# Optimization experiments

Measured on AMD Instinct MI355X. Metric: run time of the kernel, lower is better.

Reference implementation:

```python
import jax, jax.numpy as jnp
import numpy as np

D_MODEL = 1024
N_HEAD = 16
DK = D_MODEL // N_HEAD


def setup_inputs() -> dict:
    key = jax.random.key(0)
    ks = jax.random.split(key, 9)
    s = 1.0 / np.sqrt(D_MODEL)
    x = jax.random.normal(ks[0], (2, 2048, D_MODEL), dtype=jnp.float32)
    def lin(kw, kb):
        W = jax.random.uniform(kw, (D_MODEL, D_MODEL), minval=-s, maxval=s, dtype=jnp.float32)
        b = jax.random.uniform(kb, (D_MODEL,), minval=-s, maxval=s, dtype=jnp.float32)
        return W, b
    Wq, bq = lin(ks[1], ks[2])
    Wk, bk = lin(ks[3], ks[4])
    Wv, bv = lin(ks[5], ks[6])
    Wo, bo = lin(ks[7], ks[8])
    return {"x": x, "Wq": Wq, "bq": bq, "Wk": Wk, "bk": bk,
            "Wv": Wv, "bv": bv, "Wo": Wo, "bo": bo}


def reference(x, Wq, bq, Wk, bk, Wv, bv, Wo, bo):
    B, T, _ = x.shape
    # nn.Linear: x @ W.T + b; reshape to (B, H, T, dk)
    def proj(W, b):
        y = x @ W.T + b
        return y.reshape(B, T, N_HEAD, DK).transpose(0, 2, 1, 3)
    Q = proj(Wq, bq)
    K = proj(Wk, bk)
    V = proj(Wv, bv)
    scores = jnp.einsum('bhqd,bhkd->bhqk', Q, K) / jnp.sqrt(jnp.float32(DK))
    attn = jax.nn.softmax(scores, axis=-1)
    out = jnp.einsum('bhqk,bhkd->bhqd', attn, V)
    out = out.transpose(0, 2, 1, 3).reshape(B, T, D_MODEL)
    return out @ Wo.T + bo
```

## Files before the change

### kernel.cpp

```cpp
#include <hip/hip_runtime.h>
#include <hip/hip_bf16.h>
#include <cstdint>

typedef unsigned short u16;
typedef __attribute__((ext_vector_type(8))) __bf16 bf16x8;
typedef __attribute__((ext_vector_type(8))) short s16x8;
typedef __attribute__((ext_vector_type(4))) short s16x4;
typedef __attribute__((ext_vector_type(4))) float f32x4;
typedef __attribute__((ext_vector_type(4))) unsigned u32x4;

#define T_SEQ 2048
#define D_MODEL 1024
#define MROWS 4096
#define QSCALE (0.125f * 1.44269504088896f)

__device__ __forceinline__ u16 f2bf(float f) {
  unsigned u = __builtin_bit_cast(unsigned, f);
  u += 0x7fffu + ((u >> 16) & 1u);
  return (u16)(u >> 16);
}

__device__ __forceinline__ unsigned cvt_pk_bf16(float lo, float hi) {
  unsigned r;
  asm("v_cvt_pk_bf16_f32 %0, %1, %2" : "=v"(r) : "v"(lo), "v"(hi));
  return r;
}

__device__ __forceinline__ void plswap(unsigned& a, unsigned& b) {
  asm("v_permlane32_swap_b32 %0, %1" : "+v"(a), "+v"(b));
  asm("v_permlane16_swap_b32 %0, %1" : "+v"(a), "+v"(b));
}

__device__ __forceinline__ void gld_lds16(const void* g, void* l) {
  __builtin_amdgcn_global_load_lds(
      (__attribute__((address_space(1))) void*)(uintptr_t)(g),
      (__attribute__((address_space(3))) void*)(uintptr_t)(l), 16, 0, 0);
}

__device__ __forceinline__ f32x4 mfma16(s16x8 a, s16x8 b, f32x4 c) {
  return __builtin_amdgcn_mfma_f32_16x16x32_bf16(
      __builtin_bit_cast(bf16x8, a), __builtin_bit_cast(bf16x8, b), c, 0, 0, 0);
}

__global__ __launch_bounds__(256) void cvt5(
    const float* __restrict__ x,
    const float* __restrict__ w0, const float* __restrict__ w1,
    const float* __restrict__ w2, const float* __restrict__ w3,
    u16* __restrict__ dx, u16* __restrict__ dw0, u16* __restrict__ dw1,
    u16* __restrict__ dw2, u16* __restrict__ dw3) {
  const int NX = (MROWS * D_MODEL) / 4;
  const int NW = (D_MODEL * D_MODEL) / 4;
  int i = blockIdx.x * 256 + threadIdx.x;
  const float* s;
  u16* d;
  int off;
  if (i < NX) {
    s = x; d = dx; off = i;
  } else {
    int j = i - NX;
    int r = j >> 18;
    off = j & (NW - 1);
    if (r == 0) { s = w0; d = dw0; }
    else if (r == 1) { s = w1; d = dw1; }
    else if (r == 2) { s = w2; d = dw2; }
    else { s = w3; d = dw3; }
  }
  float4 v = ((const float4*)s)[off];
  uint2 o;
  o.x = cvt_pk_bf16(v.x, v.y);
  o.y = cvt_pk_bf16(v.z, v.w);
  ((uint2*)d)[off] = o;
}

__global__ __launch_bounds__(512, 2) void gemm_qkv(const u16* __restrict__ A,
    const u16* __restrict__ Wf,
    const float* __restrict__ bq, const float* __restrict__ bk, const float* __restrict__ bv,
    u16* __restrict__ Qo, u16* __restrict__ Ko, u16* __restrict__ Vo) {
  __shared__ char smem[114688];

  const int t = threadIdx.x;
  const int lane = t & 63;
  const int lq = lane & 15, g = lane >> 4;
  const int w = t >> 6;
  const int wm = w >> 2, wn = w & 3;

  const int f = blockIdx.x;
  const int xcd = f & 7, i = f >> 3;
  const int by = (xcd & 3) * 4 + (i & 3);
  const int bx = (xcd >> 2) * 8 + (i >> 2);
  const int bm2 = by * 256, bn2 = bx * 192;

  auto stage = [&](int dst, int mat, int kh, int kt2) {
    char* dbase = smem + dst * 57344;
    if (mat == 0) {
      char* lbase = dbase + kh * 16384;
#pragma unroll
      for (int s = 0; s < 2; ++s) {
        const int idx = s * 512 + t;
        const int row = idx >> 2, c16 = idx & 3;
        const int gcol = kt2 * 64 + kh * 32 + 8 * (c16 ^ ((row >> 1) & 3));
        gld_lds16(A + (size_t)(bm2 + row) * D_MODEL + gcol, lbase + idx * 16);
      }
    } else {
      char* lbase = dbase + 32768 + kh * 12288;
#pragma unroll
      for (int s = 0; s < 2; ++s) {
        const int idx = s == 0 ? t : 512 + (t & 255);
        const int row = idx >> 2, c16 = idx & 3;
        const int gcol = kt2 * 64 + kh * 32 + 8 * (c16 ^ ((row >> 1) & 3));
        gld_lds16(Wf + (size_t)(bn2 + row) * D_MODEL + gcol, lbase + idx * 16);
      }
    }
  };

  f32x4 acc[8][3] = {};
  const int swz4 = ((lq >> 1) & 3) << 4;
  const int aoff0 = (wm * 128 + lq) * 64 + ((g * 16) ^ swz4);
  const int boff0 = (wn * 48 + lq) * 64 + ((g * 16) ^ swz4);

  s16x8 bfr[3];
  auto loadB = [&](const char* cb) {
#pragma unroll
    for (int fc = 0; fc < 3; ++fc)
      bfr[fc] = *(const s16x8*)(cb + boff0 + fc * 1024);
  };
  auto quad = [&](const char* ca, int fr0) {
    s16x8 a[4];
#pragma unroll
    for (int ii = 0; ii < 4; ++ii)
      a[ii] = *(const s16x8*)(ca + aoff0 + (fr0 + ii) * 1024);
    __builtin_amdgcn_s_setprio(1);
#pragma unroll
    for (int ii = 0; ii < 4; ++ii)
#pragma unroll
      for (int fc = 0; fc < 3; ++fc)
        acc[fr0 + ii][fc] = mfma16(a[ii], bfr[fc], acc[fr0 + ii][fc]);
    __builtin_amdgcn_s_setprio(0);
  };

  stage(0, 0, 0, 0);
  stage(0, 1, 0, 0);
  stage(0, 0, 1, 0);
  stage(0, 1, 1, 0);

  const int NT = D_MODEL / 64;
#pragma unroll 1
  for (int kt = 0; kt < NT; ++kt) {
    const int d = kt & 1;
    const char* A0 = smem + d * 57344;
    const char* A1 = smem + d * 57344 + 16384;
    const char* B0 = smem + d * 57344 + 32768;
    const char* B1 = smem + d * 57344 + 32768 + 12288;
    const bool more = kt + 1 < NT;

    asm volatile("s_waitcnt vmcnt(4)" ::: "memory");
    __builtin_amdgcn_s_barrier();
    if (more) stage(d ^ 1, 0, 0, kt + 1);
    loadB(B0);
    quad(A0, 0);
    if (more) stage(d ^ 1, 1, 0, kt + 1);
    quad(A0, 4);

    if (more) asm volatile("s_waitcnt vmcnt(4)" ::: "memory");
    else      asm volatile("s_waitcnt vmcnt(0)" ::: "memory");
    __builtin_amdgcn_s_barrier();
    if (more) stage(d ^ 1, 0, 1, kt + 1);
    loadB(B1);
    quad(A1, 0);
    if (more) stage(d ^ 1, 1, 1, kt + 1);
    quad(A1, 4);
  }

#pragma unroll
  for (int fc = 0; fc < 3; ++fc) {
    const int col = bn2 + wn * 48 + fc * 16 + lq;
    const int z = col >> 10, colL = col & 1023;
    const float* bias = z == 0 ? bq : (z == 1 ? bk : bv);
    u16* out = z == 0 ? Qo : (z == 1 ? Ko : Vo);
    const float scale = z == 0 ? QSCALE : 1.0f;
    const float bvv = bias[colL];
#pragma unroll
    for (int fr = 0; fr < 8; ++fr) {
      const int row0 = bm2 + wm * 128 + fr * 16 + g * 4;
#pragma unroll
      for (int r = 0; r < 4; ++r)
        out[(size_t)(row0 + r) * D_MODEL + colL] = f2bf((acc[fr][fc][r] + bvv) * scale);
    }
  }
}

template <int BN, class Epi>
__device__ __forceinline__ void gemm_pipe(const u16* __restrict__ A,
    const u16* __restrict__ Bw, const int K, const int bm, const int bn, Epi epi) {
  constexpr int NJ = BN / 32;
  constexpr int VM = 2 + BN / 64;
  constexpr int AB = 8192;
  __shared__ char lds[3][AB + BN * 64];
  const int t = threadIdx.x;
  const int lane = t & 63;
  const int lq = lane & 15, g = lane >> 4;
  const int w = t >> 6;
  const int wr = w >> 1, wc = w & 1;

  f32x4 acc[4][NJ] = {};
  const int NT = K >> 5;

  auto stage = [&](int buf, int kt) {
    const int k0 = kt << 5;
#pragma unroll
    for (int s = 0; s < 2; ++s) {
      const int idx = s * 256 + t;
      const int kk = idx >> 7, mm = idx & 127;
      gld_lds16(A + (size_t)(bm + mm) * K + (k0 + kk * 8), &lds[buf][(idx & ~63) * 16]);
    }
#pragma unroll
    for (int s = 0; s < BN / 64; ++s) {
      const int idx = s * 256 + t;
      const int kk = idx / BN, nn = idx % BN;
      gld_lds16(Bw + (size_t)(bn + nn) * K + (k0 + kk * 8), &lds[buf][AB + (idx & ~63) * 16]);
    }
  };

  auto compute = [&](int buf) {
    const char* la = &lds[buf][0];
    const char* lb = &lds[buf][AB];
    s16x8 af[4], bfr[NJ];
#pragma unroll
    for (int i = 0; i < 4; ++i)
      af[i] = *(const s16x8*)(la + g * 2048 + (wr * 64 + i * 16 + lq) * 16);
#pragma unroll
    for (int j = 0; j < NJ; ++j)
      bfr[j] = *(const s16x8*)(lb + g * (BN * 16) + (wc * (BN / 2) + j * 16 + lq) * 16);
    __builtin_amdgcn_s_setprio(1);
#pragma unroll
    for (int i = 0; i < 4; ++i)
#pragma unroll
      for (int j = 0; j < NJ; ++j)
        acc[i][j] = mfma16(af[i], bfr[j], acc[i][j]);
    __builtin_amdgcn_s_setprio(0);
  };

  auto vmwait = [&]() {
    if constexpr (VM == 4) asm volatile("s_waitcnt vmcnt(4)" ::: "memory");
    else asm volatile("s_waitcnt vmcnt(3)" ::: "memory");
  };

  stage(0, 0);
  stage(1, 1);
  int b0 = 0, b1 = 1, b2 = 2;
#pragma unroll 1
  for (int kt = 0; kt < NT - 2; ++kt) {
    vmwait();
    __builtin_amdgcn_s_barrier();
    stage(b2, kt + 2);
    compute(b0);
    const int tmp = b0; b0 = b1; b1 = b2; b2 = tmp;
  }
  vmwait();
  __builtin_amdgcn_s_barrier();
  compute(b0);
  asm volatile("s_waitcnt vmcnt(0)" ::: "memory");
  __builtin_amdgcn_s_barrier();
  compute(b1);

  epi(acc, lq, g, wr, wc);
}

__global__ __launch_bounds__(256) void gemm_out(const u16* __restrict__ A,
    const u16* __restrict__ W, const float* __restrict__ bias, float* __restrict__ C) {
  const int f = blockIdx.x;
  const int xcd = f & 7, i = f >> 3;
  const int by = xcd * 4 + (i & 3);
  const int bx = i >> 2;
  const int bm = by * 128, bn = bx * 64;

  gemm_pipe<64>(A, W, D_MODEL, bm, bn,
      [&](f32x4 (&acc)[4][2], int lq, int g, int wr, int wc) {
#pragma unroll
        for (int j = 0; j < 2; ++j) {
          const int col = bn + wc * 32 + j * 16 + lq;
          const float bvv = bias[col];
#pragma unroll
          for (int i2 = 0; i2 < 4; ++i2) {
            const int row0 = bm + wr * 64 + i2 * 16 + g * 4;
#pragma unroll
            for (int r = 0; r < 4; ++r)
              C[(size_t)(row0 + r) * D_MODEL + col] = acc[i2][j][r] + bvv;
          }
        }
      });
}

__global__ __launch_bounds__(512, 4) void attn_kernel(const u16* __restrict__ Qw,
    const u16* __restrict__ Kw, const u16* __restrict__ Vw, u16* __restrict__ AO) {
  __shared__ char smem[73728];
  char* Ks = smem;
  char* Vs = smem + 32768;

  const int t = threadIdx.x;
  const int w = t >> 6, lane = t & 63;
  const int lq = lane & 15, g = lane >> 4;
  const int qh = w >> 1, kh = w & 1;

  const int flat = blockIdx.y * 16 + blockIdx.x;
  const int xcd = flat & 7, idx = flat >> 3;
  const int bh = xcd * 4 + (idx & 3);
  const int qt = idx >> 2;
  const int b = bh >> 4, h = bh & 15;
  const size_t headoff = (size_t)b * T_SEQ * D_MODEL + h * 64;
  const int swz = (lq & 7) << 4;

#pragma unroll
  for (int s = 0; s < 4; ++s) {
    const int u = s * 512 + t;
    const int region = u >> 9, local = u & 511;
    const int row = 64 + (local >> 5);
    *(unsigned*)(Vs + region * 10240 + 8192 + local * 4) =
        (row == 64) ? 0x3F803F80u : 0u;
  }

  s16x8 qf[2][2];
#pragma unroll
  for (int qb = 0; qb < 2; ++qb) {
    const u16* qptr = Qw + headoff + (size_t)(qt * 128 + qh * 32 + qb * 16 + lq) * D_MODEL;
#pragma unroll
    for (int hb = 0; hb < 2; ++hb)
      qf[qb][hb] = *(const s16x8*)(qptr + hb * 32 + g * 8);
  }

  auto stageK = [&](int buf, int kt) {
#pragma unroll
    for (int s = 0; s < 2; ++s) {
      const int idx2 = s * 512 + t;
      const int key = idx2 >> 3, slot = idx2 & 7;
      const int d0 = 8 * (slot ^ (key & 7));
      gld_lds16(Kw + headoff + (size_t)(kt * 128 + key) * D_MODEL + d0,
                Ks + buf * 16384 + (idx2 & ~63) * 16);
    }
  };

  const int kp = t & 63, dg = t >> 6;
  auto loadV = [&](int kt, s16x8& va, s16x8& vb2) {
    const u16* gv = Vw + headoff + (size_t)(kt * 128 + 2 * kp) * D_MODEL + 8 * dg;
    va = *(const s16x8*)gv;
    vb2 = *(const s16x8*)(gv + D_MODEL);
  };
  auto writeV = [&](int buf, s16x8 va, s16x8 vb2) {
    char* vbase = Vs + (buf * 2 + (kp >> 5)) * 10240;
    const int kpl = kp & 31;
#pragma unroll
    for (int j = 0; j < 8; ++j) {
      const int d = 8 * dg + j;
      const unsigned u = (unsigned)(u16)va[j] | ((unsigned)(u16)vb2[j] << 16);
      *(unsigned*)(vbase + d * 128 + ((4 * kpl) ^ (j << 4))) = u;
    }
  };

  f32x4 o[5][2] = {};

  s16x8 va, vb2;
  stageK(0, 0);
  loadV(0, va, vb2);

  int cur = 0;
#pragma unroll 1
  for (int kt = 0; kt < T_SEQ / 128; ++kt) {
    asm volatile("s_waitcnt vmcnt(0)" ::: "memory");
    writeV(cur, va, vb2);
    __syncthreads();
    const bool more = kt + 1 < T_SEQ / 128;
    if (more) { stageK(cur ^ 1, kt + 1); loadV(kt + 1, va, vb2); }

#pragma unroll
    for (int ks = 0; ks < 2; ++ks) {
      const char* kb_ = Ks + cur * 16384 + (ks * 64 + kh * 32) * 128;
      f32x4 s[2][2] = {};
      __builtin_amdgcn_s_setprio(1);
#pragma unroll
      for (int kb = 0; kb < 2; ++kb)
#pragma unroll
        for (int hb = 0; hb < 2; ++hb) {
          const s16x8 kf = *(const s16x8*)(kb_ + (16 * kb + lq) * 128 + ((64 * hb + 16 * g) ^ swz));
#pragma unroll
          for (int qb = 0; qb < 2; ++qb)
            s[kb][qb] = mfma16(kf, qf[qb][hb], s[kb][qb]);
        }
      __builtin_amdgcn_s_setprio(0);

#pragma unroll
      for (int kb = 0; kb < 2; ++kb)
#pragma unroll
        for (int qb = 0; qb < 2; ++qb)
#pragma unroll
          for (int r = 0; r < 4; ++r) s[kb][qb][r] = __builtin_amdgcn_exp2f(s[kb][qb][r]);

      s16x8 pb[2];
#pragma unroll
      for (int qb = 0; qb < 2; ++qb) {
        unsigned a0 = cvt_pk_bf16(s[0][qb][0], s[0][qb][1]);
        unsigned a1 = cvt_pk_bf16(s[0][qb][2], s[0][qb][3]);
        unsigned b0 = cvt_pk_bf16(s[1][qb][0], s[1][qb][1]);
        unsigned b1 = cvt_pk_bf16(s[1][qb][2], s[1][qb][3]);
        plswap(a0, b0);
        plswap(a1, b1);
        u32x4 pk = {a0, a1, b0, b1};
        pb[qb] = __builtin_bit_cast(s16x8, pk);
      }

      const char* vb_ = Vs + (cur * 2 + ks) * 10240;
      __builtin_amdgcn_s_setprio(1);
#pragma unroll
      for (int f = 0; f < 5; ++f) {
        const s16x8 av = *(const s16x8*)(vb_ + (16 * f + lq) * 128 +
                                         ((64 * kh + 16 * g) ^ swz));
#pragma unroll
        for (int qb = 0; qb < 2; ++qb)
          o[f][qb] = mfma16(av, pb[qb], o[f][qb]);
      }
      __builtin_amdgcn_s_setprio(0);
    }
    cur ^= 1;
  }

  float rsq[2];
#pragma unroll
  for (int qb = 0; qb < 2; ++qb)
    rsq[qb] = __shfl(o[4][qb][0], lq);

  __syncthreads();
  char* obuf = smem;
  float* rbuf = (float*)(smem + 32768);
  if (kh == 1) {
#pragma unroll
    for (int f = 0; f < 4; ++f)
#pragma unroll
      for (int qb = 0; qb < 2; ++qb)
        *(f32x4*)(obuf + qh * 8192 + lane * 128 + (((f * 2 + qb) * 16) ^ ((lane & 7) << 4))) =
            o[f][qb];
    rbuf[qh * 128 + lane * 2 + 0] = rsq[0];
    rbuf[qh * 128 + lane * 2 + 1] = rsq[1];
  }
  __syncthreads();
  if (kh == 0) {
#pragma unroll
    for (int f = 0; f < 4; ++f)
#pragma unroll
      for (int qb = 0; qb < 2; ++qb)
        o[f][qb] += *(const f32x4*)(obuf + qh * 8192 + lane * 128 +
                                    (((f * 2 + qb) * 16) ^ ((lane & 7) << 4)));
    const float inv0 = 1.0f / (rsq[0] + rbuf[qh * 128 + lane * 2 + 0]);
    const float inv1 = 1.0f / (rsq[1] + rbuf[qh * 128 + lane * 2 + 1]);
#pragma unroll
    for (int qb = 0; qb < 2; ++qb) {
      const float inv = qb ? inv1 : inv0;
      u16* orow = AO + headoff + (size_t)(qt * 128 + qh * 32 + qb * 16 + lq) * D_MODEL;
#pragma unroll
      for (int f = 0; f < 4; ++f) {
        uint2 ov;
        ov.x = cvt_pk_bf16(o[f][qb][0] * inv, o[f][qb][1] * inv);
        ov.y = cvt_pk_bf16(o[f][qb][2] * inv, o[f][qb][3] * inv);
        *(uint2*)(orow + 16 * f + 4 * g) = ov;
      }
    }
  }
}

extern "C" void kernel_launch(void* const* d_in, const int* in_sizes, int n_in,
                              void* d_out, int out_size, void* d_ws, size_t ws_size,
                              hipStream_t stream) {
  const float* x  = (const float*)d_in[0];
  const float* Wq = (const float*)d_in[1];
  const float* bq = (const float*)d_in[2];
  const float* Wk = (const float*)d_in[3];
  const float* bk = (const float*)d_in[4];
  const float* Wv = (const float*)d_in[5];
  const float* bv = (const float*)d_in[6];
  const float* Wo = (const float*)d_in[7];
  const float* bo = (const float*)d_in[8];

  char* ws = (char*)d_ws;
  const size_t MB = 1u << 20;
  u16* x_bf  = (u16*)(ws + 0 * MB);
  u16* AO    = x_bf;
  u16* Wq_bf = (u16*)(ws + 8 * MB);
  u16* Wk_bf = (u16*)(ws + 10 * MB);
  u16* Wv_bf = (u16*)(ws + 12 * MB);
  u16* Wo_bf = (u16*)(ws + 14 * MB);
  u16* Qs  = (u16*)(ws + 16 * MB);
  u16* Ksb = (u16*)(ws + 24 * MB);
  u16* Vsb = (u16*)(ws + 32 * MB);

  const int NCVT = (MROWS * D_MODEL + 4 * D_MODEL * D_MODEL) / 4;
  cvt5<<<NCVT / 256, 256, 0, stream>>>(x, Wq, Wk, Wv, Wo,
                                       x_bf, Wq_bf, Wk_bf, Wv_bf, Wo_bf);

  gemm_qkv<<<256, 512, 0, stream>>>(x_bf, Wq_bf, bq, bk, bv, Qs, Ksb, Vsb);
  attn_kernel<<<dim3(16, 32), 512, 0, stream>>>(Qs, Ksb, Vsb, AO);
  gemm_out<<<512, 256, 0, stream>>>(AO, Wo_bf, bo, (float*)d_out);
}
```

Measured before the change: 113.7 us.

## Use 256x256 QKV GEMM tiles with deeper half-K prefetch schedule

Changes the QKV projection tiles from 256x192 to 256x256, so the grid shrinks from 256 to 192 blocks and each wave computes 8x4 MFMA fragments. The K loop is restructured so loads are staged two half-steps ahead, with barriers wrapped around each MFMA cluster. Because a tile never spans two of the Q/K/V outputs, the per-column bias and output selection is hoisted. The aim is more reuse per load and better overlap of loads with MFMAs, at the cost of 128KB of LDS (one block per CU), more accumulator registers, more barriers, and 192 blocks that may not fill all 256 CUs.

```diff
diff --git a/kernel.cpp b/kernel.cpp
--- a/kernel.cpp
+++ b/kernel.cpp
@@ -76,7 +76,7 @@
     const u16* __restrict__ Wf,
     const float* __restrict__ bq, const float* __restrict__ bk, const float* __restrict__ bv,
     u16* __restrict__ Qo, u16* __restrict__ Ko, u16* __restrict__ Vo) {
-  __shared__ char smem[114688];
+  __shared__ char smem[131072];
 
   const int t = threadIdx.x;
   const int lane = t & 63;
@@ -87,104 +87,112 @@
   const int f = blockIdx.x;
   const int xcd = f & 7, i = f >> 3;
   const int by = (xcd & 3) * 4 + (i & 3);
-  const int bx = (xcd >> 2) * 8 + (i >> 2);
-  const int bm2 = by * 256, bn2 = bx * 192;
-
-  auto stage = [&](int dst, int mat, int kh, int kt2) {
-    char* dbase = smem + dst * 57344;
-    if (mat == 0) {
-      char* lbase = dbase + kh * 16384;
-#pragma unroll
-      for (int s = 0; s < 2; ++s) {
-        const int idx = s * 512 + t;
-        const int row = idx >> 2, c16 = idx & 3;
-        const int gcol = kt2 * 64 + kh * 32 + 8 * (c16 ^ ((row >> 1) & 3));
-        gld_lds16(A + (size_t)(bm2 + row) * D_MODEL + gcol, lbase + idx * 16);
-      }
-    } else {
-      char* lbase = dbase + 32768 + kh * 12288;
-#pragma unroll
-      for (int s = 0; s < 2; ++s) {
-        const int idx = s == 0 ? t : 512 + (t & 255);
-        const int row = idx >> 2, c16 = idx & 3;
-        const int gcol = kt2 * 64 + kh * 32 + 8 * (c16 ^ ((row >> 1) & 3));
-        gld_lds16(Wf + (size_t)(bn2 + row) * D_MODEL + gcol, lbase + idx * 16);
-      }
-    }
-  };
-
-  f32x4 acc[8][3] = {};
+  const int bx = (xcd >> 2) * 6 + (i >> 2);
+  const int bm2 = by * 256, bn2 = bx * 256;
+
+  auto chunk = [&](int kt, int mat, int kh) -> char* {
+    return smem + (kt & 1) * 65536 + mat * 32768 + kh * 16384;
+  };
+
+  auto stage = [&](int mat, int kh, int kt2) {
+    const u16* gbase = mat ? Wf : A;
+    const int gr0 = mat ? bn2 : bm2;
+    char* lbase = chunk(kt2, mat, kh);
+#pragma unroll
+    for (int s = 0; s < 2; ++s) {
+      const int idx = s * 512 + t;
+      const int row = idx >> 2, c16 = idx & 3;
+      const int gcol = kt2 * 64 + kh * 32 + 8 * (c16 ^ ((row >> 1) & 3));
+      gld_lds16(gbase + (size_t)(gr0 + row) * D_MODEL + gcol, lbase + idx * 16);
+    }
+  };
+
+  f32x4 acc[8][4] = {};
   const int swz4 = ((lq >> 1) & 3) << 4;
   const int aoff0 = (wm * 128 + lq) * 64 + ((g * 16) ^ swz4);
-  const int boff0 = (wn * 48 + lq) * 64 + ((g * 16) ^ swz4);
-
-  s16x8 bfr[3];
-  auto loadB = [&](const char* cb) {
-#pragma unroll
-    for (int fc = 0; fc < 3; ++fc)
+  const int boff0 = (wn * 64 + lq) * 64 + ((g * 16) ^ swz4);
+
+  s16x8 bfr[4];
+  s16x8 a[4];
+
+  auto readB = [&](const char* cb) {
+#pragma unroll
+    for (int fc = 0; fc < 4; ++fc)
       bfr[fc] = *(const s16x8*)(cb + boff0 + fc * 1024);
   };
-  auto quad = [&](const char* ca, int fr0) {
-    s16x8 a[4];
+  auto readA = [&](const char* ca, int fr0) {
 #pragma unroll
     for (int ii = 0; ii < 4; ++ii)
       a[ii] = *(const s16x8*)(ca + aoff0 + (fr0 + ii) * 1024);
+  };
+  auto cluster = [&](int fr0) {
     __builtin_amdgcn_s_setprio(1);
 #pragma unroll
     for (int ii = 0; ii < 4; ++ii)
 #pragma unroll
-      for (int fc = 0; fc < 3; ++fc)
+      for (int fc = 0; fc < 4; ++fc)
         acc[fr0 + ii][fc] = mfma16(a[ii], bfr[fc], acc[fr0 + ii][fc]);
     __builtin_amdgcn_s_setprio(0);
   };
 
-  stage(0, 0, 0, 0);
-  stage(0, 1, 0, 0);
-  stage(0, 0, 1, 0);
-  stage(0, 1, 1, 0);
-
-  const int NT = D_MODEL / 64;
+  stage(0, 0, 0); stage(1, 0, 0); stage(0, 1, 0); stage(1, 1, 0);
+  stage(0, 0, 1); stage(1, 0, 1);
+  asm volatile("s_waitcnt vmcnt(4)" ::: "memory");
+  __builtin_amdgcn_s_barrier();
+
+  const int NT = 16;
 #pragma unroll 1
   for (int kt = 0; kt < NT; ++kt) {
-    const int d = kt & 1;
-    const char* A0 = smem + d * 57344;
-    const char* A1 = smem + d * 57344 + 16384;
-    const char* B0 = smem + d * 57344 + 32768;
-    const char* B1 = smem + d * 57344 + 32768 + 12288;
-    const bool more = kt + 1 < NT;
-
-    asm volatile("s_waitcnt vmcnt(4)" ::: "memory");
-    __builtin_amdgcn_s_barrier();
-    if (more) stage(d ^ 1, 0, 0, kt + 1);
-    loadB(B0);
-    quad(A0, 0);
-    if (more) stage(d ^ 1, 1, 0, kt + 1);
-    quad(A0, 4);
-
-    if (more) asm volatile("s_waitcnt vmcnt(4)" ::: "memory");
-    else      asm volatile("s_waitcnt vmcnt(0)" ::: "memory");
-    __builtin_amdgcn_s_barrier();
-    if (more) stage(d ^ 1, 0, 1, kt + 1);
-    loadB(B1);
-    quad(A1, 0);
-    if (more) stage(d ^ 1, 1, 1, kt + 1);
-    quad(A1, 4);
-  }
-
-#pragma unroll
-  for (int fc = 0; fc < 3; ++fc) {
-    const int col = bn2 + wn * 48 + fc * 16 + lq;
-    const int z = col >> 10, colL = col & 1023;
-    const float* bias = z == 0 ? bq : (z == 1 ? bk : bv);
-    u16* out = z == 0 ? Qo : (z == 1 ? Ko : Vo);
-    const float scale = z == 0 ? QSCALE : 1.0f;
-    const float bvv = bias[colL];
+    const char* A0 = chunk(kt, 0, 0);
+    const char* A1 = chunk(kt, 0, 1);
+    const char* B0 = chunk(kt, 1, 0);
+    const char* B1 = chunk(kt, 1, 1);
+    const bool s1 = kt + 1 < NT, s2 = kt + 2 < NT;
+
+    readB(B0);
+    readA(A0, 0);
+    if (s1) stage(0, 1, kt + 1);
+    __builtin_amdgcn_s_barrier();
+    cluster(0);
+    __builtin_amdgcn_s_barrier();
+
+    readA(A0, 4);
+    if (s1) stage(1, 1, kt + 1);
+    __builtin_amdgcn_s_barrier();
+    cluster(4);
+    __builtin_amdgcn_s_barrier();
+
+    readB(B1);
+    readA(A1, 0);
+    if (s2) stage(0, 0, kt + 2);
+    __builtin_amdgcn_s_barrier();
+    cluster(0);
+    __builtin_amdgcn_s_barrier();
+
+    readA(A1, 4);
+    if (s2) stage(1, 0, kt + 2);
+    __builtin_amdgcn_s_barrier();
+    cluster(4);
+    if (s2) asm volatile("s_waitcnt vmcnt(4)" ::: "memory");
+    else    asm volatile("s_waitcnt vmcnt(0)" ::: "memory");
+    __builtin_amdgcn_s_barrier();
+  }
+
+  const int z = bn2 >> 10;
+  const float* bias = z == 0 ? bq : (z == 1 ? bk : bv);
+  u16* out = z == 0 ? Qo : (z == 1 ? Ko : Vo);
+  const float scale = z == 0 ? QSCALE : 1.0f;
+  const int bnl = bn2 & 1023;
+#pragma unroll
+  for (int fc = 0; fc < 4; ++fc) {
+    const int col = bnl + wn * 64 + fc * 16 + lq;
+    const float bvv = bias[col];
 #pragma unroll
     for (int fr = 0; fr < 8; ++fr) {
       const int row0 = bm2 + wm * 128 + fr * 16 + g * 4;
 #pragma unroll
       for (int r = 0; r < 4; ++r)
-        out[(size_t)(row0 + r) * D_MODEL + colL] = f2bf((acc[fr][fc][r] + bvv) * scale);
+        out[(size_t)(row0 + r) * D_MODEL + col] = f2bf((acc[fr][fc][r] + bvv) * scale);
     }
   }
 }
@@ -494,7 +502,7 @@
   cvt5<<<NCVT / 256, 256, 0, stream>>>(x, Wq, Wk, Wv, Wo,
                                        x_bf, Wq_bf, Wk_bf, Wv_bf, Wo_bf);
 
-  gemm_qkv<<<256, 512, 0, stream>>>(x_bf, Wq_bf, bq, bk, bv, Qs, Ksb, Vsb);
+  gemm_qkv<<<192, 512, 0, stream>>>(x_bf, Wq_bf, bq, bk, bv, Qs, Ksb, Vsb);
   attn_kernel<<<dim3(16, 32), 512, 0, stream>>>(Qs, Ksb, Vsb, AO);
   gemm_out<<<512, 256, 0, stream>>>(AO, Wo_bf, bo, (float*)d_out);
 }
```

Measured after the change: 117.6 us. 3.4% more time.

## Restructure output projection GEMM with 256x64 tiles, swizzled LDS and double buffering

Applied to the files above, without the earlier changes.

Replaces the generic triple-buffered 128x64 GEMM used for the output projection with a dedicated kernel using 256x64 block tiles, 512 threads, and a K-step of 64 split into two half-stages. Loads go into an XOR-swizzled LDS layout to reduce bank conflicts, and the next tile's loads are interleaved between MFMA groups. The aim is more reuse of each weight tile and fewer LDS conflicts. In exchange the kernel uses more LDS per block, launches fewer blocks, and uses only two buffers, which may expose more load latency.

```diff
diff --git a/kernel.cpp b/kernel.cpp
--- a/kernel.cpp
+++ b/kernel.cpp
@@ -189,106 +189,112 @@
   }
 }
 
-template <int BN, class Epi>
-__device__ __forceinline__ void gemm_pipe(const u16* __restrict__ A,
-    const u16* __restrict__ Bw, const int K, const int bm, const int bn, Epi epi) {
-  constexpr int NJ = BN / 32;
-  constexpr int VM = 2 + BN / 64;
-  constexpr int AB = 8192;
-  __shared__ char lds[3][AB + BN * 64];
+__global__ __launch_bounds__(512, 2) void gemm_out(const u16* __restrict__ A,
+    const u16* __restrict__ W, const float* __restrict__ bias, float* __restrict__ C) {
+  __shared__ char smem[81920];
+
   const int t = threadIdx.x;
   const int lane = t & 63;
   const int lq = lane & 15, g = lane >> 4;
   const int w = t >> 6;
-  const int wr = w >> 1, wc = w & 1;
-
-  f32x4 acc[4][NJ] = {};
-  const int NT = K >> 5;
-
-  auto stage = [&](int buf, int kt) {
-    const int k0 = kt << 5;
-#pragma unroll
-    for (int s = 0; s < 2; ++s) {
-      const int idx = s * 256 + t;
-      const int kk = idx >> 7, mm = idx & 127;
-      gld_lds16(A + (size_t)(bm + mm) * K + (k0 + kk * 8), &lds[buf][(idx & ~63) * 16]);
-    }
-#pragma unroll
-    for (int s = 0; s < BN / 64; ++s) {
-      const int idx = s * 256 + t;
-      const int kk = idx / BN, nn = idx % BN;
-      gld_lds16(Bw + (size_t)(bn + nn) * K + (k0 + kk * 8), &lds[buf][AB + (idx & ~63) * 16]);
-    }
-  };
-
-  auto compute = [&](int buf) {
-    const char* la = &lds[buf][0];
-    const char* lb = &lds[buf][AB];
-    s16x8 af[4], bfr[NJ];
-#pragma unroll
-    for (int i = 0; i < 4; ++i)
-      af[i] = *(const s16x8*)(la + g * 2048 + (wr * 64 + i * 16 + lq) * 16);
-#pragma unroll
-    for (int j = 0; j < NJ; ++j)
-      bfr[j] = *(const s16x8*)(lb + g * (BN * 16) + (wc * (BN / 2) + j * 16 + lq) * 16);
-    __builtin_amdgcn_s_setprio(1);
-#pragma unroll
-    for (int i = 0; i < 4; ++i)
-#pragma unroll
-      for (int j = 0; j < NJ; ++j)
-        acc[i][j] = mfma16(af[i], bfr[j], acc[i][j]);
-    __builtin_amdgcn_s_setprio(0);
-  };
-
-  auto vmwait = [&]() {
-    if constexpr (VM == 4) asm volatile("s_waitcnt vmcnt(4)" ::: "memory");
-    else asm volatile("s_waitcnt vmcnt(3)" ::: "memory");
-  };
-
-  stage(0, 0);
-  stage(1, 1);
-  int b0 = 0, b1 = 1, b2 = 2;
-#pragma unroll 1
-  for (int kt = 0; kt < NT - 2; ++kt) {
-    vmwait();
-    __builtin_amdgcn_s_barrier();
-    stage(b2, kt + 2);
-    compute(b0);
-    const int tmp = b0; b0 = b1; b1 = b2; b2 = tmp;
-  }
-  vmwait();
-  __builtin_amdgcn_s_barrier();
-  compute(b0);
-  asm volatile("s_waitcnt vmcnt(0)" ::: "memory");
-  __builtin_amdgcn_s_barrier();
-  compute(b1);
-
-  epi(acc, lq, g, wr, wc);
-}
-
-__global__ __launch_bounds__(256) void gemm_out(const u16* __restrict__ A,
-    const u16* __restrict__ W, const float* __restrict__ bias, float* __restrict__ C) {
+  const int wm = w >> 1, wn = w & 1;
+
   const int f = blockIdx.x;
   const int xcd = f & 7, i = f >> 3;
-  const int by = xcd * 4 + (i & 3);
-  const int bx = i >> 2;
-  const int bm = by * 128, bn = bx * 64;
-
-  gemm_pipe<64>(A, W, D_MODEL, bm, bn,
-      [&](f32x4 (&acc)[4][2], int lq, int g, int wr, int wc) {
-#pragma unroll
-        for (int j = 0; j < 2; ++j) {
-          const int col = bn + wc * 32 + j * 16 + lq;
-          const float bvv = bias[col];
-#pragma unroll
-          for (int i2 = 0; i2 < 4; ++i2) {
-            const int row0 = bm + wr * 64 + i2 * 16 + g * 4;
-#pragma unroll
-            for (int r = 0; r < 4; ++r)
-              C[(size_t)(row0 + r) * D_MODEL + col] = acc[i2][j][r] + bvv;
-          }
-        }
-      });
+  const int by = (xcd & 3) * 4 + (i & 3);
+  const int bx = (xcd >> 2) * 8 + (i >> 2);
+  const int bm2 = by * 256, bn2 = bx * 64;
+
+  auto stage = [&](int dst, int mat, int kh, int kt2) {
+    char* dbase = smem + dst * 40960;
+    if (mat == 0) {
+      char* lbase = dbase + kh * 16384;
+#pragma unroll
+      for (int s = 0; s < 2; ++s) {
+        const int idx = s * 512 + t;
+        const int row = idx >> 2, c16 = idx & 3;
+        const int gcol = kt2 * 64 + kh * 32 + 8 * (c16 ^ ((row >> 1) & 3));
+        gld_lds16(A + (size_t)(bm2 + row) * D_MODEL + gcol, lbase + idx * 16);
+      }
+    } else {
+      char* lbase = dbase + 32768 + kh * 4096;
+      const int idx = t & 255;
+      const int row = idx >> 2, c16 = idx & 3;
+      const int gcol = kt2 * 64 + kh * 32 + 8 * (c16 ^ ((row >> 1) & 3));
+      gld_lds16(W + (size_t)(bn2 + row) * D_MODEL + gcol, lbase + idx * 16);
+    }
+  };
+
+  f32x4 acc[4][2] = {};
+  const int swz4 = ((lq >> 1) & 3) << 4;
+  const int aoff0 = (wm * 64 + lq) * 64 + ((g * 16) ^ swz4);
+  const int boff0 = (wn * 32 + lq) * 64 + ((g * 16) ^ swz4);
+
+  s16x8 bfr[2];
+  auto loadB = [&](const char* cb) {
+#pragma unroll
+    for (int fc = 0; fc < 2; ++fc)
+      bfr[fc] = *(const s16x8*)(cb + boff0 + fc * 1024);
+  };
+  auto quad = [&](const char* ca, int fr0) {
+    s16x8 a[2];
+#pragma unroll
+    for (int ii = 0; ii < 2; ++ii)
+      a[ii] = *(const s16x8*)(ca + aoff0 + (fr0 + ii) * 1024);
+    __builtin_amdgcn_s_setprio(1);
+#pragma unroll
+    for (int ii = 0; ii < 2; ++ii)
+#pragma unroll
+      for (int fc = 0; fc < 2; ++fc)
+        acc[fr0 + ii][fc] = mfma16(a[ii], bfr[fc], acc[fr0 + ii][fc]);
+    __builtin_amdgcn_s_setprio(0);
+  };
+
+  stage(0, 0, 0, 0);
+  stage(0, 1, 0, 0);
+  stage(0, 0, 1, 0);
+  stage(0, 1, 1, 0);
+
+  const int NT = D_MODEL / 64;
+#pragma unroll 1
+  for (int kt = 0; kt < NT; ++kt) {
+    const int d = kt & 1;
+    const char* A0 = smem + d * 40960;
+    const char* A1 = smem + d * 40960 + 16384;
+    const char* B0 = smem + d * 40960 + 32768;
+    const char* B1 = smem + d * 40960 + 32768 + 4096;
+    const bool more = kt + 1 < NT;
+
+    asm volatile("s_waitcnt vmcnt(3)" ::: "memory");
+    __builtin_amdgcn_s_barrier();
+    if (more) stage(d ^ 1, 0, 0, kt + 1);
+    loadB(B0);
+    quad(A0, 0);
+    if (more) stage(d ^ 1, 1, 0, kt + 1);
+    quad(A0, 2);
+
+    if (more) asm volatile("s_waitcnt vmcnt(3)" ::: "memory");
+    else      asm volatile("s_waitcnt vmcnt(0)" ::: "memory");
+    __builtin_amdgcn_s_barrier();
+    if (more) stage(d ^ 1, 0, 1, kt + 1);
+    loadB(B1);
+    quad(A1, 0);
+    if (more) stage(d ^ 1, 1, 1, kt + 1);
+    quad(A1, 2);
+  }
+
+#pragma unroll
+  for (int fc = 0; fc < 2; ++fc) {
+    const int col = bn2 + wn * 32 + fc * 16 + lq;
+    const float bvv = bias[col];
+#pragma unroll
+    for (int fr = 0; fr < 4; ++fr) {
+      const int row0 = bm2 + wm * 64 + fr * 16 + g * 4;
+#pragma unroll
+      for (int r = 0; r < 4; ++r)
+        C[(size_t)(row0 + r) * D_MODEL + col] = acc[fr][fc][r] + bvv;
+    }
+  }
 }
 
 __global__ __launch_bounds__(512, 4) void attn_kernel(const u16* __restrict__ Qw,
@@ -496,5 +502,5 @@
 
   gemm_qkv<<<256, 512, 0, stream>>>(x_bf, Wq_bf, bq, bk, bv, Qs, Ksb, Vsb);
   attn_kernel<<<dim3(16, 32), 512, 0, stream>>>(Qs, Ksb, Vsb, AO);
-  gemm_out<<<512, 256, 0, stream>>>(AO, Wo_bf, bo, (float*)d_out);
-}
+  gemm_out<<<256, 512, 0, stream>>>(AO, Wo_bf, bo, (float*)d_out);
+}
```

After: 103.3 us (median of 3 runs). 1.1x faster.
